# Optimization experiments

Hardware: AMD Instinct MI355X
Metric: run time of the kernel (lower is better)

## Reference

```python
import jax, jax.numpy as jnp
import numpy as np
from jax import lax

D_MODEL = 1024
D_INNER = 2048
B = 8
T = 2048
INIT_ALPHA_BIAS = 2.0


def setup_inputs() -> dict:
    key = jax.random.key(0)
    ks = jax.random.split(key, 6)
    def xavier(k, shape):
        fan_in, fan_out = shape[1], shape[0]
        lim = float(np.sqrt(6.0 / (fan_in + fan_out)))
        return jax.random.uniform(k, shape, jnp.float32, -lim, lim)
    return {
        "x": jax.random.normal(ks[0], (B, T, D_MODEL), jnp.float32),
        "h0": jnp.zeros((B, D_INNER), jnp.float32),
        "W_in": xavier(ks[1], (D_INNER, D_MODEL)),
        "W_alpha": xavier(ks[2], (D_INNER, D_INNER)),
        "b_alpha": jnp.full((D_INNER,), INIT_ALPHA_BIAS, jnp.float32),
        "W_v": xavier(ks[3], (D_INNER, D_INNER)),
        "b_v": jnp.zeros((D_INNER,), jnp.float32),
        "W_out": xavier(ks[4], (D_MODEL, D_INNER)),
    }


def reference(x, h0, W_in, W_alpha, b_alpha, W_v, b_v, W_out):
    # in_proj + silu pre-activation: [B,T,D_inner]
    x_proj = jax.nn.silu(jnp.einsum('btd,id->bti', x, W_in))
    # time-major for the scan: [T,B,D_inner]
    xr = jnp.transpose(x_proj, (1, 0, 2))
    # precompute gate and value for all steps (big GEMMs)
    alpha = jax.nn.sigmoid(jnp.einsum('tbd,ed->tbe', xr, W_alpha) + b_alpha)
    v = jnp.einsum('tbd,ed->tbe', xr, W_v) + b_v

    def step(h, av):
        a, vt = av
        h_new = a * h + (1.0 - a) * vt  # decay-gated update
        out_t = h_new * jax.nn.silu(h_new)  # self-gating
        return h_new, out_t

    h_final, outs = lax.scan(step, h0, (alpha, v))  # outs: [T,B,D_inner]
    # out_proj back to model dim, batch-major: [B,T,D_model]
    output = jnp.einsum('tbe,de->btd', outs, W_out)
    return output, h_final
```

## Files before the change

kernel.cpp:

```cpp
#include <hip/hip_runtime.h>
#include <cstdint>
#include <cstddef>

typedef unsigned short u16;
typedef unsigned int   u32;

#define D_MODEL 1024
#define D_INNER 2048
#define BATCH   8
#define TSEQ    2048
#define MROWS   (BATCH*TSEQ)
#define CHUNK   32
#define NCHUNK  (TSEQ/CHUNK)
#define EDIM    (BATCH*D_INNER)

typedef float  f32x4  __attribute__((ext_vector_type(4)));
typedef __bf16 bf16x8 __attribute__((ext_vector_type(8)));
typedef short  s16x8  __attribute__((ext_vector_type(8)));

__device__ __forceinline__ float bf2f(u16 u){ return __builtin_bit_cast(float, (u32)u << 16); }
__device__ __forceinline__ u16 f2bf(float f){
  u32 u = __builtin_bit_cast(u32, f);
  u += 0x7fffu + ((u >> 16) & 1u);
  return (u16)(u >> 16);
}
__device__ __forceinline__ float sigm(float x){ return 1.0f/(1.0f + __expf(-x)); }

__device__ __forceinline__ void gld16(const u16* g, u16* l){
  __builtin_amdgcn_global_load_lds((const __attribute__((address_space(1))) void*)g,
                                   (__attribute__((address_space(3))) void*)l, 16, 0, 0);
}

__device__ __forceinline__ s16x8 cvt8(const float* s){
  float4 u0 = *(const float4*)s;
  float4 u1 = *(const float4*)(s + 4);
  s16x8 p;
  p[0]=(short)f2bf(u0.x); p[1]=(short)f2bf(u0.y);
  p[2]=(short)f2bf(u0.z); p[3]=(short)f2bf(u0.w);
  p[4]=(short)f2bf(u1.x); p[5]=(short)f2bf(u1.y);
  p[6]=(short)f2bf(u1.z); p[7]=(short)f2bf(u1.w);
  return p;
}

template<int MODE, int K, int N, bool BA, bool BB>
__global__ __launch_bounds__(256) void gemm_bt(
    const void* __restrict__ Ap, const void* __restrict__ Bp,
    const float* __restrict__ bias, void* __restrict__ Cout)
{
  __shared__ __align__(16) u16 sA[128*32];
  __shared__ __align__(16) u16 sB[128*32];
  const int tid = threadIdx.x;
  const int bm = blockIdx.x, bn = blockIdx.y;
  const int w = tid >> 6, lane = tid & 63;
  const int wr = w >> 1, wc = w & 1;
  const int l15 = lane & 15, kg = lane >> 4;

  const int r0   = tid >> 2;
  const int koff = (tid & 3) * 8;

  int ga[2];
  #pragma unroll
  for (int i = 0; i < 2; ++i){
    int mc = bm*128 + r0 + i*64;
    if (MODE == 0)      ga[i] = (mc & 7) * TSEQ + (mc >> 3);
    else if (MODE == 3) ga[i] = (mc & (TSEQ-1)) * BATCH + (mc >> 11);
    else                ga[i] = mc;
  }

  const u16*   Abf = (const u16*)Ap;
  const float* Af  = (const float*)Ap;
  const u16*   Bbf = (const u16*)Bp;
  const float* Bf  = (const float*)Bp;

  u16* la[2] = { sA + w*512, sA + 2048 + w*512 };
  u16* lb[2] = { sB + w*512, sB + 2048 + w*512 };
  u16* ldsA = sA + tid*8;
  u16* ldsB = sB + tid*8;

  const int gb[2] = { bn*128 + r0, bn*128 + r0 + 64 };

  f32x4 acc[4][4] = {};

  for (int kt = 0; kt < K/32; ++kt){
    __syncthreads();
    if constexpr (BA){
      gld16(Abf + (size_t)ga[0]*K + koff + kt*32, la[0]);
      gld16(Abf + (size_t)ga[1]*K + koff + kt*32, la[1]);
    } else {
      #pragma unroll
      for (int i = 0; i < 2; ++i)
        *(s16x8*)(ldsA + i*2048) = cvt8(Af + (size_t)ga[i]*K + koff + kt*32);
    }
    if constexpr (BB){
      gld16(Bbf + (size_t)gb[0]*K + koff + kt*32, lb[0]);
      gld16(Bbf + (size_t)gb[1]*K + koff + kt*32, lb[1]);
    } else {
      #pragma unroll
      for (int i = 0; i < 2; ++i)
        *(s16x8*)(ldsB + i*2048) = cvt8(Bf + (size_t)gb[i]*K + koff + kt*32);
    }
    __syncthreads();

    s16x8 af[4], bfr[4];
    #pragma unroll
    for (int m = 0; m < 4; ++m)
      af[m] = *(const s16x8*)(sA + (wr*64 + m*16 + l15)*32 + kg*8);
    #pragma unroll
    for (int n = 0; n < 4; ++n)
      bfr[n] = *(const s16x8*)(sB + (wc*64 + n*16 + l15)*32 + kg*8);
    #pragma unroll
    for (int m = 0; m < 4; ++m)
      #pragma unroll
      for (int n = 0; n < 4; ++n)
        acc[m][n] = __builtin_amdgcn_mfma_f32_16x16x32_bf16(
            __builtin_bit_cast(bf16x8, af[m]),
            __builtin_bit_cast(bf16x8, bfr[n]),
            acc[m][n], 0, 0, 0);
  }

  #pragma unroll
  for (int m = 0; m < 4; ++m){
    #pragma unroll
    for (int n = 0; n < 4; ++n){
      #pragma unroll
      for (int r = 0; r < 4; ++r){
        const int row = bm*128 + wr*64 + m*16 + kg*4 + r;
        const int col = bn*128 + wc*64 + n*16 + l15;
        float val = acc[m][n][r];
        if constexpr (MODE == 0){
          val = val * sigm(val);
          ((u16*)Cout)[(size_t)row*N + col] = f2bf(val);
        } else if constexpr (MODE == 1){
          val = sigm(val + bias[col]);
          ((u16*)Cout)[(size_t)row*N + col] = f2bf(val);
        } else if constexpr (MODE == 2){
          val = val + bias[col];
          ((u16*)Cout)[(size_t)row*N + col] = f2bf(val);
        } else {
          ((float*)Cout)[(size_t)row*N + col] = val;
        }
      }
    }
  }
}

__global__ __launch_bounds__(256) void scan_pass1(
    const u16* __restrict__ alpha, const u16* __restrict__ v,
    float* __restrict__ P, float* __restrict__ H)
{
  const int e = blockIdx.x*256 + threadIdx.x;
  const int c = blockIdx.y;
  const size_t base = (size_t)c*CHUNK*EDIM + e;
  float p = 1.f, h = 0.f;
  #pragma unroll 8
  for (int t = 0; t < CHUNK; ++t){
    float a  = bf2f(alpha[base + (size_t)t*EDIM]);
    float vv = bf2f(v[base + (size_t)t*EDIM]);
    p *= a;
    h = a*h + (1.f - a)*vv;
  }
  P[(size_t)c*EDIM + e] = p;
  H[(size_t)c*EDIM + e] = h;
}

__global__ __launch_bounds__(256) void scan_pass2(
    const float* __restrict__ P, const float* __restrict__ H,
    const float* __restrict__ h0, float* __restrict__ hstart,
    float* __restrict__ hfinal)
{
  const int e = blockIdx.x*256 + threadIdx.x;
  float hs = h0[e];
  for (int c = 0; c < NCHUNK; ++c){
    hstart[(size_t)c*EDIM + e] = hs;
    hs = P[(size_t)c*EDIM + e]*hs + H[(size_t)c*EDIM + e];
  }
  hfinal[e] = hs;
}

__global__ __launch_bounds__(256) void scan_pass3(
    const u16* __restrict__ alpha, const u16* __restrict__ v,
    const float* __restrict__ hstart, u16* __restrict__ outs)
{
  const int e = blockIdx.x*256 + threadIdx.x;
  const int c = blockIdx.y;
  const size_t base = (size_t)c*CHUNK*EDIM + e;
  float h = hstart[(size_t)c*EDIM + e];
  #pragma unroll 8
  for (int t = 0; t < CHUNK; ++t){
    float a  = bf2f(alpha[base + (size_t)t*EDIM]);
    float vv = bf2f(v[base + (size_t)t*EDIM]);
    h = a*h + (1.f - a)*vv;
    float o = h*h*sigm(h);
    outs[base + (size_t)t*EDIM] = f2bf(o);
  }
}

__global__ __launch_bounds__(256) void cvt_bf16(
    const float* __restrict__ src, u16* __restrict__ dst, int n4)
{
  const int i = blockIdx.x*256 + threadIdx.x;
  if (i >= n4) return;
  const float4 f = ((const float4*)src)[i];
  u32 w0 = (u32)f2bf(f.x) | ((u32)f2bf(f.y) << 16);
  u32 w1 = (u32)f2bf(f.z) | ((u32)f2bf(f.w) << 16);
  ((uint2*)dst)[i] = make_uint2(w0, w1);
}

extern "C" void kernel_launch(void* const* d_in, const int* in_sizes, int n_in,
                              void* d_out, int out_size, void* d_ws, size_t ws_size,
                              hipStream_t stream)
{
  const float* x     = (const float*)d_in[0];
  const float* h0    = (const float*)d_in[1];
  const float* W_in  = (const float*)d_in[2];
  const float* W_al  = (const float*)d_in[3];
  const float* b_al  = (const float*)d_in[4];
  const float* W_v   = (const float*)d_in[5];
  const float* b_v   = (const float*)d_in[6];
  const float* W_out = (const float*)d_in[7];

  float* out  = (float*)d_out;
  float* hfin = out + (size_t)MROWS*D_MODEL;

  const size_t SZ_ACT = (size_t)MROWS*D_INNER*2;
  const size_t SZ_ST  = (size_t)NCHUNK*EDIM*4;
  const size_t SZ_WI  = (size_t)D_INNER*D_MODEL*2;
  const size_t SZ_WA  = (size_t)D_INNER*D_INNER*2;
  const size_t need_min  = 3*SZ_ACT + 3*SZ_ST;
  const size_t need_fast = need_min + 2*SZ_WI + 2*SZ_WA + 8192;

  if (ws_size < need_min) return;

  char* ws = (char*)d_ws;
  auto carve = [&](size_t bytes){
    char* p = ws; ws += (bytes + 255) & ~(size_t)255; return p;
  };
  u16* xp   = (u16*)carve(SZ_ACT);
  u16* alp  = (u16*)carve(SZ_ACT);
  u16* vv   = (u16*)carve(SZ_ACT);
  float* P  = (float*)carve(SZ_ST);
  float* H  = (float*)carve(SZ_ST);
  float* hs = (float*)carve(SZ_ST);

  const dim3 gBig(MROWS/128, D_INNER/128);
  const dim3 gOut(MROWS/128, D_MODEL/128);
  const dim3 gScan(EDIM/256, NCHUNK);

  auto cvt = [&](const float* s, u16* d, size_t n){
    int n4 = (int)(n/4);
    cvt_bf16<<<(n4+255)/256, 256, 0, stream>>>(s, d, n4);
  };

  if (ws_size >= need_fast){
    u16* wib = (u16*)carve(SZ_WI);
    u16* wab = (u16*)carve(SZ_WA);
    u16* wvb = (u16*)carve(SZ_WA);
    u16* wob = (u16*)carve(SZ_WI);
    u16* xb  = alp;

    cvt(x,     xb,  (size_t)MROWS*D_MODEL);
    cvt(W_in,  wib, (size_t)D_INNER*D_MODEL);
    cvt(W_al,  wab, (size_t)D_INNER*D_INNER);
    cvt(W_v,   wvb, (size_t)D_INNER*D_INNER);
    cvt(W_out, wob, (size_t)D_MODEL*D_INNER);

    gemm_bt<0, D_MODEL, D_INNER, true, true><<<gBig, 256, 0, stream>>>(xb, wib, nullptr, xp);
    gemm_bt<1, D_INNER, D_INNER, true, true><<<gBig, 256, 0, stream>>>(xp, wab, b_al,    alp);
    gemm_bt<2, D_INNER, D_INNER, true, true><<<gBig, 256, 0, stream>>>(xp, wvb, b_v,     vv);

    scan_pass1<<<gScan, 256, 0, stream>>>(alp, vv, P, H);
    scan_pass2<<<EDIM/256, 256, 0, stream>>>(P, H, h0, hs, hfin);
    scan_pass3<<<gScan, 256, 0, stream>>>(alp, vv, hs, vv);

    gemm_bt<3, D_INNER, D_MODEL, true, true><<<gOut, 256, 0, stream>>>(vv, wob, nullptr, out);
  } else {
    gemm_bt<0, D_MODEL, D_INNER, false, false><<<gBig, 256, 0, stream>>>(x,  W_in, nullptr, xp);
    gemm_bt<1, D_INNER, D_INNER, true,  false><<<gBig, 256, 0, stream>>>(xp, W_al, b_al,    alp);
    gemm_bt<2, D_INNER, D_INNER, true,  false><<<gBig, 256, 0, stream>>>(xp, W_v,  b_v,     vv);

    scan_pass1<<<gScan, 256, 0, stream>>>(alp, vv, P, H);
    scan_pass2<<<EDIM/256, 256, 0, stream>>>(P, H, h0, hs, hfin);
    scan_pass3<<<gScan, 256, 0, stream>>>(alp, vv, hs, vv);

    gemm_bt<3, D_INNER, D_MODEL, true, false><<<gOut, 256, 0, stream>>>(vv, W_out, nullptr, out);
  }
}
```

Measured before the change: 640.2 us.

## Replace GEMMs with 256x256 double-buffered swizzled-LDS MFMA kernel and time-major x

Adds a new GEMM kernel with 256x256 tiles, 512 threads, K-step 64, double-buffered LDS staging via global_load_lds overlapped with MFMA, an XOR swizzle against bank conflicts, and setprio around the MFMA blocks. The input x is now converted to bf16 directly in time-major order, so the GEMMs no longer need gathered row indexing. The output GEMM scatters rows back to batch-major in its epilogue. The intent is higher arithmetic intensity and less load latency in the four large GEMMs, at the cost of more registers and LDS per block and fewer blocks in the grid.

```diff
diff --git a/kernel.cpp b/kernel.cpp
--- a/kernel.cpp
+++ b/kernel.cpp
@@ -42,6 +42,124 @@
   return p;
 }
 
+template<int MODE, int K, int N>
+__global__ __launch_bounds__(512, 2) void gemm256(
+    const u16* __restrict__ A, const u16* __restrict__ Bt,
+    const float* __restrict__ bias, void* __restrict__ Cout)
+{
+  __shared__ __align__(16) u16 sAB[2][2][16384];
+  constexpr int NT = K/64;
+  const int tid = threadIdx.x;
+  const int w = tid >> 6, lane = tid & 63;
+  const int wr = w >> 2, wc = w & 3;
+  const int l15 = lane & 15, kg = lane >> 4;
+  const int bm = blockIdx.x, bn = blockIdx.y;
+
+  const int st_row8 = w*8 + (lane>>3);
+  const int st_colb = ((lane&7)*16) ^ (((lane>>5)&1)<<5);
+  const size_t a_base = (size_t)(bm*256) * K + (st_colb>>1);
+  const size_t b_base = (size_t)(bn*256) * K + (st_colb>>1);
+
+  auto stageA = [&](int buf, int kt, int upper){
+    u16* dst = &sAB[0][buf][upper*8192 + w*512];
+    #pragma unroll
+    for (int i = 0; i < 2; ++i){
+      int row = upper*128 + i*64 + st_row8;
+      gld16(A + a_base + (size_t)row*K + kt*64, dst + i*4096);
+    }
+  };
+  auto stageB = [&](int buf, int kt, int upper){
+    u16* dst = &sAB[1][buf][upper*8192 + w*512];
+    #pragma unroll
+    for (int i = 0; i < 2; ++i){
+      int row = upper*128 + i*64 + st_row8;
+      gld16(Bt + b_base + (size_t)row*K + kt*64, dst + i*4096);
+    }
+  };
+
+  const int sw   = ((l15>>2)&1)<<5;
+  const int rdA0 = ((wr*128 + l15)*128 + kg*16) ^ sw;
+  const int rdB0 = ((wc*64  + l15)*128 + kg*16) ^ sw;
+
+  f32x4 acc[8][4] = {};
+
+  stageA(0, 0, 0); stageB(0, 0, 0); stageA(0, 0, 1); stageB(0, 0, 1);
+  asm volatile("s_waitcnt vmcnt(4)" ::: "memory");
+  __builtin_amdgcn_s_barrier();
+
+  for (int t = 0; t < NT; ++t){
+    const char* As = (const char*)&sAB[0][t&1][0];
+    const char* Bs = (const char*)&sAB[1][t&1][0];
+    const int nb = (t+1)&1;
+    const bool more = (t < NT-1);
+    #pragma unroll
+    for (int q = 0; q < 4; ++q){
+      const int mh = (q>>1) ^ (q&1);
+      const int nh = q>>1;
+      s16x8 af[4][2], bf[2][2];
+      #pragma unroll
+      for (int mf = 0; mf < 4; ++mf)
+        #pragma unroll
+        for (int ks = 0; ks < 2; ++ks)
+          af[mf][ks] = *(const s16x8*)(As + rdA0 + mh*8192 + mf*2048 + ks*64);
+      #pragma unroll
+      for (int nf = 0; nf < 2; ++nf)
+        #pragma unroll
+        for (int ks = 0; ks < 2; ++ks)
+          bf[nf][ks] = *(const s16x8*)(Bs + rdB0 + nh*4096 + nf*2048 + ks*64);
+      if (more){
+        if      (q == 0) stageA(nb, t+1, 0);
+        else if (q == 1) stageB(nb, t+1, 0);
+        else if (q == 2) stageA(nb, t+1, 1);
+        else             stageB(nb, t+1, 1);
+        asm volatile("s_waitcnt vmcnt(4)" ::: "memory");
+      } else {
+        asm volatile("s_waitcnt vmcnt(0)" ::: "memory");
+      }
+      __builtin_amdgcn_s_barrier();
+      __builtin_amdgcn_s_setprio(1);
+      #pragma unroll
+      for (int mf = 0; mf < 4; ++mf)
+        #pragma unroll
+        for (int nf = 0; nf < 2; ++nf)
+          #pragma unroll
+          for (int ks = 0; ks < 2; ++ks)
+            acc[mh*4+mf][nh*2+nf] = __builtin_amdgcn_mfma_f32_16x16x32_bf16(
+                __builtin_bit_cast(bf16x8, af[mf][ks]),
+                __builtin_bit_cast(bf16x8, bf[nf][ks]),
+                acc[mh*4+mf][nh*2+nf], 0, 0, 0);
+      __builtin_amdgcn_s_setprio(0);
+      __builtin_amdgcn_s_barrier();
+    }
+  }
+
+  #pragma unroll
+  for (int mi = 0; mi < 8; ++mi){
+    #pragma unroll
+    for (int ni = 0; ni < 4; ++ni){
+      #pragma unroll
+      for (int r = 0; r < 4; ++r){
+        const int row = bm*256 + wr*128 + mi*16 + kg*4 + r;
+        const int col = bn*256 + wc*64 + ni*16 + l15;
+        float val = acc[mi][ni][r];
+        if constexpr (MODE == 0){
+          val = val * sigm(val);
+          ((u16*)Cout)[(size_t)row*N + col] = f2bf(val);
+        } else if constexpr (MODE == 1){
+          val = sigm(val + bias[col]);
+          ((u16*)Cout)[(size_t)row*N + col] = f2bf(val);
+        } else if constexpr (MODE == 2){
+          val = val + bias[col];
+          ((u16*)Cout)[(size_t)row*N + col] = f2bf(val);
+        } else {
+          const int orow = (row & 7)*TSEQ + (row >> 3);
+          ((float*)Cout)[(size_t)orow*N + col] = val;
+        }
+      }
+    }
+  }
+}
+
 template<int MODE, int K, int N, bool BA, bool BB>
 __global__ __launch_bounds__(256) void gemm_bt(
     const void* __restrict__ Ap, const void* __restrict__ Bp,
@@ -54,7 +172,6 @@
   const int w = tid >> 6, lane = tid & 63;
   const int wr = w >> 1, wc = w & 1;
   const int l15 = lane & 15, kg = lane >> 4;
-
   const int r0   = tid >> 2;
   const int koff = (tid & 3) * 8;
 
@@ -66,21 +183,17 @@
     else if (MODE == 3) ga[i] = (mc & (TSEQ-1)) * BATCH + (mc >> 11);
     else                ga[i] = mc;
   }
-
   const u16*   Abf = (const u16*)Ap;
   const float* Af  = (const float*)Ap;
   const u16*   Bbf = (const u16*)Bp;
   const float* Bf  = (const float*)Bp;
-
   u16* la[2] = { sA + w*512, sA + 2048 + w*512 };
   u16* lb[2] = { sB + w*512, sB + 2048 + w*512 };
   u16* ldsA = sA + tid*8;
   u16* ldsB = sB + tid*8;
-
   const int gb[2] = { bn*128 + r0, bn*128 + r0 + 64 };
 
   f32x4 acc[4][4] = {};
-
   for (int kt = 0; kt < K/32; ++kt){
     __syncthreads();
     if constexpr (BA){
@@ -117,11 +230,10 @@
             __builtin_bit_cast(bf16x8, bfr[n]),
             acc[m][n], 0, 0, 0);
   }
-
   #pragma unroll
-  for (int m = 0; m < 4; ++m){
-    #pragma unroll
-    for (int n = 0; n < 4; ++n){
+  for (int m = 0; m < 4; ++m)
+    #pragma unroll
+    for (int n = 0; n < 4; ++n)
       #pragma unroll
       for (int r = 0; r < 4; ++r){
         const int row = bm*128 + wr*64 + m*16 + kg*4 + r;
@@ -140,8 +252,6 @@
           ((float*)Cout)[(size_t)row*N + col] = val;
         }
       }
-    }
-  }
 }
 
 __global__ __launch_bounds__(256) void scan_pass1(
@@ -206,6 +316,20 @@
   ((uint2*)dst)[i] = make_uint2(w0, w1);
 }
 
+__global__ __launch_bounds__(256) void cvt_x_tm(
+    const float* __restrict__ src, u16* __restrict__ dst)
+{
+  const int i = blockIdx.x*256 + threadIdx.x;
+  const int d4  = i & 255;
+  const int rin = i >> 8;
+  const int b = rin >> 11, tt = rin & (TSEQ-1);
+  const int rout = tt*BATCH + b;
+  const float4 f = ((const float4*)src)[i];
+  u32 w0 = (u32)f2bf(f.x) | ((u32)f2bf(f.y) << 16);
+  u32 w1 = (u32)f2bf(f.z) | ((u32)f2bf(f.w) << 16);
+  ((uint2*)dst)[(size_t)rout*256 + d4] = make_uint2(w0, w1);
+}
+
 extern "C" void kernel_launch(void* const* d_in, const int* in_sizes, int n_in,
                               void* d_out, int out_size, void* d_ws, size_t ws_size,
                               hipStream_t stream)
@@ -242,8 +366,6 @@
   float* H  = (float*)carve(SZ_ST);
   float* hs = (float*)carve(SZ_ST);
 
-  const dim3 gBig(MROWS/128, D_INNER/128);
-  const dim3 gOut(MROWS/128, D_MODEL/128);
   const dim3 gScan(EDIM/256, NCHUNK);
 
   auto cvt = [&](const float* s, u16* d, size_t n){
@@ -258,22 +380,24 @@
     u16* wob = (u16*)carve(SZ_WI);
     u16* xb  = alp;
 
-    cvt(x,     xb,  (size_t)MROWS*D_MODEL);
+    cvt_x_tm<<<(MROWS*D_MODEL/4)/256, 256, 0, stream>>>(x, xb);
     cvt(W_in,  wib, (size_t)D_INNER*D_MODEL);
     cvt(W_al,  wab, (size_t)D_INNER*D_INNER);
     cvt(W_v,   wvb, (size_t)D_INNER*D_INNER);
     cvt(W_out, wob, (size_t)D_MODEL*D_INNER);
 
-    gemm_bt<0, D_MODEL, D_INNER, true, true><<<gBig, 256, 0, stream>>>(xb, wib, nullptr, xp);
-    gemm_bt<1, D_INNER, D_INNER, true, true><<<gBig, 256, 0, stream>>>(xp, wab, b_al,    alp);
-    gemm_bt<2, D_INNER, D_INNER, true, true><<<gBig, 256, 0, stream>>>(xp, wvb, b_v,     vv);
+    gemm256<0, D_MODEL, D_INNER><<<dim3(MROWS/256, D_INNER/256), 512, 0, stream>>>(xb, wib, nullptr, xp);
+    gemm256<1, D_INNER, D_INNER><<<dim3(MROWS/256, D_INNER/256), 512, 0, stream>>>(xp, wab, b_al,    alp);
+    gemm256<2, D_INNER, D_INNER><<<dim3(MROWS/256, D_INNER/256), 512, 0, stream>>>(xp, wvb, b_v,     vv);
 
     scan_pass1<<<gScan, 256, 0, stream>>>(alp, vv, P, H);
     scan_pass2<<<EDIM/256, 256, 0, stream>>>(P, H, h0, hs, hfin);
     scan_pass3<<<gScan, 256, 0, stream>>>(alp, vv, hs, vv);
 
-    gemm_bt<3, D_INNER, D_MODEL, true, true><<<gOut, 256, 0, stream>>>(vv, wob, nullptr, out);
+    gemm256<3, D_INNER, D_MODEL><<<dim3(MROWS/256, D_MODEL/256), 512, 0, stream>>>(vv, wob, nullptr, out);
   } else {
+    const dim3 gBig(MROWS/128, D_INNER/128);
+    const dim3 gOut(MROWS/128, D_MODEL/128);
     gemm_bt<0, D_MODEL, D_INNER, false, false><<<gBig, 256, 0, stream>>>(x,  W_in, nullptr, xp);
     gemm_bt<1, D_INNER, D_INNER, true,  false><<<gBig, 256, 0, stream>>>(xp, W_al, b_al,    alp);
     gemm_bt<2, D_INNER, D_INNER, true,  false><<<gBig, 256, 0, stream>>>(xp, W_v,  b_v,     vv);
```

Result: faster. 617.0 us (-3.6%).
